# Kernel tuning notes

Measured on AMD Instinct MI355X. Metric: run time of the kernel, lower is better.

Reference implementation:

```python
import jax, jax.numpy as jnp
import numpy as np

N, E, NFEAT, HID, HEADS, NCLASS = 100000, 1600000, 256, 64, 1, 32


def gat_conv(x, src, dst, W, a_src, a_dst, b, H, C, concat):
    n = x.shape[0]
    h = (x @ W).reshape(n, H, C)                      # [N,H,C]
    a_s = (h * a_src).sum(-1)                          # [N,H]
    a_d = (h * a_dst).sum(-1)                          # [N,H]
    e = jax.nn.leaky_relu(a_s[src] + a_d[dst], 0.2)    # [E,H]
    emax = jax.ops.segment_max(e, dst, num_segments=n)
    emax = jnp.where(jnp.isfinite(emax), emax, 0.0)
    ex = jnp.exp(e - emax[dst])
    denom = jax.ops.segment_sum(ex, dst, num_segments=n)
    alpha = ex / (denom[dst] + 1e-16)                  # segment softmax over in-edges of dst
    msg = h[src] * alpha[:, :, None]                   # [E,H,C]
    out = jax.ops.segment_sum(msg, dst, num_segments=n)
    out = out.reshape(n, H * C) if concat else out.mean(axis=1)
    return out + b


def setup_inputs() -> dict:
    key = jax.random.key(0)
    ks = jax.random.split(key, 14)
    x = jax.random.normal(ks[0], (N, NFEAT), dtype=jnp.float32)
    edge_index = jax.random.randint(ks[1], (2, E), 0, N, dtype=jnp.int64)
    s = 0.05
    return {
        'x': x, 'edge_index': edge_index,
        'W1': jax.random.normal(ks[2], (NFEAT, HEADS * HID), jnp.float32) * s,
        'as1': jax.random.normal(ks[3], (HEADS, HID), jnp.float32) * s,
        'ad1': jax.random.normal(ks[4], (HEADS, HID), jnp.float32) * s,
        'b1': jnp.zeros((HEADS * HID,), jnp.float32),
        'W2': jax.random.normal(ks[5], (HEADS * HID, HEADS * HID), jnp.float32) * s,
        'as2': jax.random.normal(ks[6], (HEADS, HID), jnp.float32) * s,
        'ad2': jax.random.normal(ks[7], (HEADS, HID), jnp.float32) * s,
        'b2': jnp.zeros((HEADS * HID,), jnp.float32),
        'W3': jax.random.normal(ks[8], (HEADS * HID, HEADS * NCLASS), jnp.float32) * s,
        'as3': jax.random.normal(ks[9], (HEADS, NCLASS), jnp.float32) * s,
        'ad3': jax.random.normal(ks[10], (HEADS, NCLASS), jnp.float32) * s,
        'b3': jnp.zeros((NCLASS,), jnp.float32),
    }


def reference(x, edge_index, W1, as1, ad1, b1, W2, as2, ad2, b2, W3, as3, ad3, b3):
    # add self loops (PyG GATConv add_self_loops=True)
    loop = jnp.arange(N, dtype=edge_index.dtype)
    src = jnp.concatenate([edge_index[0], loop])
    dst = jnp.concatenate([edge_index[1], loop])
    out = jax.nn.leaky_relu(gat_conv(x, src, dst, W1, as1, ad1, b1, HEADS, HID, True), 0.01)
    out = jax.nn.leaky_relu(gat_conv(out, src, dst, W2, as2, ad2, b2, HEADS, HID, True), 0.01)
    out = gat_conv(out, src, dst, W3, as3, ad3, b3, HEADS, NCLASS, False)
    return out
```

## Files before the change

### kernel.cpp

```cpp
#include <hip/hip_runtime.h>

#define NN 100000
#define NE 1600000
#define NF 256
#define HD 64
#define NC 32

#define BKS 8
#define NBK ((NN + 255) >> 8)
#define CHUNK 4096
#define NBLK ((NE + CHUNK - 1) / CHUNK)

__device__ __forceinline__ float lrelu02(float x) { return fmaxf(x, 0.2f * x); }

typedef __attribute__((ext_vector_type(8))) short bf16x8;
typedef __attribute__((ext_vector_type(4))) float f32x4;
typedef __attribute__((ext_vector_type(4))) _Float16 f16x4;

__device__ __forceinline__ unsigned short f2bf(float f) {
    unsigned int u = __float_as_uint(f);
    unsigned int r = u + 0x7FFFu + ((u >> 16) & 1u);
    return (unsigned short)(r >> 16);
}
__device__ __forceinline__ float bf2f(unsigned short s) {
    return __uint_as_float(((unsigned int)s) << 16);
}
__device__ __forceinline__ void split4(float4 v, uint2& hi, uint2& lo) {
    unsigned short h0 = f2bf(v.x), h1 = f2bf(v.y), h2 = f2bf(v.z), h3 = f2bf(v.w);
    unsigned short l0 = f2bf(v.x - bf2f(h0)), l1 = f2bf(v.y - bf2f(h1));
    unsigned short l2 = f2bf(v.z - bf2f(h2)), l3 = f2bf(v.w - bf2f(h3));
    hi.x = (unsigned int)h0 | ((unsigned int)h1 << 16);
    hi.y = (unsigned int)h2 | ((unsigned int)h3 << 16);
    lo.x = (unsigned int)l0 | ((unsigned int)l1 << 16);
    lo.y = (unsigned int)l2 | ((unsigned int)l3 << 16);
}


__global__ __launch_bounds__(256) void bucket_hist(const int* __restrict__ dst, int* __restrict__ gcnt) {
    __shared__ int hist[NBK];
    int tid = threadIdx.x;
    for (int i = tid; i < NBK; i += 256) hist[i] = 0;
    __syncthreads();
    int base = blockIdx.x * CHUNK;
    #pragma unroll
    for (int k = 0; k < CHUNK / 256; k++) {
        int i = base + k * 256 + tid;
        if (i < NE) atomicAdd(&hist[dst[i] >> BKS], 1);
    }
    __syncthreads();
    for (int i = tid; i < NBK; i += 256) if (hist[i]) atomicAdd(&gcnt[i], hist[i]);
}

__global__ void bucket_scan(const int* __restrict__ gcnt, int* __restrict__ gbase, int* __restrict__ gcur) {
    __shared__ int sh[512];
    int tid = threadIdx.x;
    int v = (tid < NBK) ? gcnt[tid] : 0;
    sh[tid] = v;
    __syncthreads();
    for (int d = 1; d < 512; d <<= 1) {
        int t = (tid >= d) ? sh[tid - d] : 0;
        __syncthreads();
        sh[tid] += t;
        __syncthreads();
    }
    if (tid < NBK) { int ex = sh[tid] - v; gbase[tid] = ex; gcur[tid] = ex; }
}

__global__ __launch_bounds__(256) void bin_edges(const int* __restrict__ src, const int* __restrict__ dst,
                                                 int* __restrict__ gcur, int2* __restrict__ ebuf) {
    __shared__ int hist[NBK];
    __shared__ int excl[NBK];
    __shared__ int runbase[NBK];
    __shared__ int ssum[256];
    __shared__ int2 sorted[CHUNK];
    int tid = threadIdx.x;
    int base = blockIdx.x * CHUNK;
    int n = NE - base; if (n > CHUNK) n = CHUNK;

    for (int i = tid; i < NBK; i += 256) hist[i] = 0;
    __syncthreads();

    int2 ed[CHUNK / 256];
    int bk[CHUNK / 256];
    #pragma unroll
    for (int k = 0; k < CHUNK / 256; k++) {
        int i = base + k * 256 + tid;
        if (i < NE) {
            ed[k] = make_int2(src[i], dst[i]);
            bk[k] = ed[k].y >> BKS;
            atomicAdd(&hist[bk[k]], 1);
        } else bk[k] = -1;
    }
    __syncthreads();
    int h0 = (2 * tid < NBK) ? hist[2 * tid] : 0;
    int h1 = (2 * tid + 1 < NBK) ? hist[2 * tid + 1] : 0;
    ssum[tid] = h0 + h1;
    __syncthreads();
    for (int d = 1; d < 256; d <<= 1) {
        int t = (tid >= d) ? ssum[tid - d] : 0;
        __syncthreads();
        ssum[tid] += t;
        __syncthreads();
    }
    int pref = ssum[tid] - (h0 + h1);
    if (2 * tid < NBK) excl[2 * tid] = pref;
    if (2 * tid + 1 < NBK) excl[2 * tid + 1] = pref + h0;
    for (int b = tid; b < NBK; b += 256) {
        int c = hist[b];
        runbase[b] = c ? atomicAdd(&gcur[b], c) : 0;
    }
    __syncthreads();
    #pragma unroll
    for (int k = 0; k < CHUNK / 256; k++) {
        if (bk[k] >= 0) {
            int r = atomicAdd(&excl[bk[k]], 1);
            sorted[r] = ed[k];
        }
    }
    __syncthreads();
    for (int i = tid; i < n; i += 256) {
        int2 e = sorted[i];
        int b = e.y >> BKS;
        int local_rank = i - (excl[b] - hist[b]);
        ebuf[runbase[b] + local_rank] = e;
    }
}

__global__ __launch_bounds__(256) void bucket_csr(const int2* __restrict__ ebuf, const int* __restrict__ gbase,
                                                  const int* __restrict__ gcnt,
                                                  int* __restrict__ offs, int* __restrict__ csr) {
    __shared__ int hist[256], cur[256], ssum[256];
    int b = blockIdx.x, tid = threadIdx.x;
    int ebeg = gbase[b], cnt = gcnt[b];
    int node0 = b << BKS;
    hist[tid] = 0;
    __syncthreads();
    for (int i = ebeg + tid; i < ebeg + cnt; i += 256)
        atomicAdd(&hist[ebuf[i].y & 255], 1);
    __syncthreads();
    int v = hist[tid];
    ssum[tid] = v;
    __syncthreads();
    for (int d = 1; d < 256; d <<= 1) {
        int t = (tid >= d) ? ssum[tid - d] : 0;
        __syncthreads();
        ssum[tid] += t;
        __syncthreads();
    }
    int ex = ebeg + ssum[tid] - v;
    cur[tid] = ex;
    int nnode = NN - node0; if (nnode > 256) nnode = 256;
    if (tid < nnode) offs[node0 + tid] = ex;
    if (b == NBK - 1 && tid == nnode - 1) offs[NN] = ebeg + cnt;
    __syncthreads();
    for (int i = ebeg + tid; i < ebeg + cnt; i += 256) {
        int2 e = ebuf[i];
        int pos = atomicAdd(&cur[e.y & 255], 1);
        csr[pos] = e.x;
    }
}


template <int CIN, int COUT>
__global__ __launch_bounds__(256) void mfma_gemm(const float* __restrict__ in, const float* __restrict__ W,
                                                 const float* __restrict__ a_s, const float* __restrict__ a_d,
                                                 _Float16* __restrict__ hout, float* __restrict__ asv,
                                                 float* __restrict__ adv) {
    const int KC  = 32;
    const int BM  = 128;
    const int NCT = COUT / 16;
    const int NCH = CIN / KC;
    const int TPC = 256 / COUT;
    const int KPER = KC / TPC;

    __shared__ unsigned short Ah[2][4 * BM * 8];
    __shared__ unsigned short Al[2][4 * BM * 8];
    __shared__ unsigned short Bh[2][4 * COUT * 8];
    __shared__ unsigned short Bl[2][4 * COUT * 8];

    int tid  = threadIdx.x;
    int lane = tid & 63;
    int wave = tid >> 6;
    int fr = lane & 15;
    int kg = lane >> 4;
    int n0base = blockIdx.x * BM;

    int wcol = tid % COUT;
    int kseg = tid / COUT;
    int kb   = kseg * KPER;
    int kgW  = kb >> 3;
    int kofW = kb & 7;

    float4 xr[4];
    float  wreg[KPER];

    f32x4 acc[2][NCT];
    #pragma unroll
    for (int rt = 0; rt < 2; rt++)
        #pragma unroll
        for (int ct = 0; ct < NCT; ct++) acc[rt][ct] = (f32x4){0.f, 0.f, 0.f, 0.f};

    auto load_regs = [&](int k0) {
        #pragma unroll
        for (int i = 0; i < 4; i++) {
            int f = tid + i * 256;
            int row = f >> 3, q = f & 7;
            int gn = n0base + row;
            xr[i] = make_float4(0.f, 0.f, 0.f, 0.f);
            if (gn < NN) xr[i] = *(const float4*)&in[(size_t)gn * CIN + k0 + q * 4];
        }
        #pragma unroll
        for (int j = 0; j < KPER; j++)
            wreg[j] = W[(size_t)(k0 + kb + j) * COUT + wcol];
    };

    auto write_lds = [&](int buf) {
        #pragma unroll
        for (int i = 0; i < 4; i++) {
            int f = tid + i * 256;
            int row = f >> 3, q = f & 7;
            int akg = q >> 1, off = (q & 1) * 4;
            uint2 hi, lo;
            split4(xr[i], hi, lo);
            *(uint2*)&Ah[buf][(akg * BM + row) * 8 + off] = hi;
            *(uint2*)&Al[buf][(akg * BM + row) * 8 + off] = lo;
        }
        unsigned short bh8[8], bl8[8];
        #pragma unroll
        for (int j = 0; j < KPER; j++) {
            bh8[j] = f2bf(wreg[j]);
            bl8[j] = f2bf(wreg[j] - bf2f(bh8[j]));
        }
        if constexpr (KPER == 8) {
            uint4 ph = make_uint4((unsigned)bh8[0] | ((unsigned)bh8[1] << 16), (unsigned)bh8[2] | ((unsigned)bh8[3] << 16),
                                  (unsigned)bh8[4] | ((unsigned)bh8[5] << 16), (unsigned)bh8[6] | ((unsigned)bh8[7] << 16));
            uint4 pl = make_uint4((unsigned)bl8[0] | ((unsigned)bl8[1] << 16), (unsigned)bl8[2] | ((unsigned)bl8[3] << 16),
                                  (unsigned)bl8[4] | ((unsigned)bl8[5] << 16), (unsigned)bl8[6] | ((unsigned)bl8[7] << 16));
            *(uint4*)&Bh[buf][(kgW * COUT + wcol) * 8 + kofW] = ph;
            *(uint4*)&Bl[buf][(kgW * COUT + wcol) * 8 + kofW] = pl;
        } else {
            uint2 ph = make_uint2((unsigned)bh8[0] | ((unsigned)bh8[1] << 16), (unsigned)bh8[2] | ((unsigned)bh8[3] << 16));
            uint2 pl = make_uint2((unsigned)bl8[0] | ((unsigned)bl8[1] << 16), (unsigned)bl8[2] | ((unsigned)bl8[3] << 16));
            *(uint2*)&Bh[buf][(kgW * COUT + wcol) * 8 + kofW] = ph;
            *(uint2*)&Bl[buf][(kgW * COUT + wcol) * 8 + kofW] = pl;
        }
    };

    auto do_mfma = [&](int buf) {
        bf16x8 ah[2], al[2];
        #pragma unroll
        for (int rt = 0; rt < 2; rt++) {
            int row = wave * 32 + rt * 16 + fr;
            ah[rt] = *(const bf16x8*)&Ah[buf][(kg * BM + row) * 8];
            al[rt] = *(const bf16x8*)&Al[buf][(kg * BM + row) * 8];
        }
        #pragma unroll
        for (int ct = 0; ct < NCT; ct++) {
            int col = ct * 16 + fr;
            bf16x8 bh = *(const bf16x8*)&Bh[buf][(kg * COUT + col) * 8];
            bf16x8 bl = *(const bf16x8*)&Bl[buf][(kg * COUT + col) * 8];
            #pragma unroll
            for (int rt = 0; rt < 2; rt++) {
                acc[rt][ct] = __builtin_amdgcn_mfma_f32_16x16x32_bf16(ah[rt], bh, acc[rt][ct], 0, 0, 0);
                acc[rt][ct] = __builtin_amdgcn_mfma_f32_16x16x32_bf16(ah[rt], bl, acc[rt][ct], 0, 0, 0);
                acc[rt][ct] = __builtin_amdgcn_mfma_f32_16x16x32_bf16(al[rt], bh, acc[rt][ct], 0, 0, 0);
            }
        }
    };

    load_regs(0);
    write_lds(0);
    __syncthreads();

    for (int t = 0; t < NCH; t++) {
        int cur = t & 1;
        if (t + 1 < NCH) load_regs((t + 1) * KC);
        do_mfma(cur);
        if (t + 1 < NCH) {
            write_lds(cur ^ 1);
            __syncthreads();
        }
    }

    float As_l[NCT], Ad_l[NCT];
    #pragma unroll
    for (int ct = 0; ct < NCT; ct++) {
        As_l[ct] = a_s[ct * 16 + fr];
        Ad_l[ct] = a_d[ct * 16 + fr];
    }
    #pragma unroll
    for (int rt = 0; rt < 2; rt++) {
        #pragma unroll
        for (int r = 0; r < 4; r++) {
            int row = n0base + wave * 32 + rt * 16 + kg * 4 + r;
            if (row < NN) {
                #pragma unroll
                for (int ct = 0; ct < NCT; ct++)
                    hout[(size_t)row * COUT + ct * 16 + fr] = (_Float16)acc[rt][ct][r];
            }
            float ps = 0.f, pd = 0.f;
            #pragma unroll
            for (int ct = 0; ct < NCT; ct++) {
                ps += acc[rt][ct][r] * As_l[ct];
                pd += acc[rt][ct][r] * Ad_l[ct];
            }
            #pragma unroll
            for (int off = 1; off < 16; off <<= 1) {
                ps += __shfl_xor(ps, off);
                pd += __shfl_xor(pd, off);
            }
            if (fr == 0 && row < NN) { asv[row] = ps; adv[row] = pd; }
        }
    }
}


template <int C, bool ACT>
__global__ __launch_bounds__(256) void gat_agg(const _Float16* __restrict__ h16, const float* __restrict__ asv,
                                               const float* __restrict__ adv, const int* __restrict__ offs,
                                               const int* __restrict__ csr,
                                               const float* __restrict__ bias, float* __restrict__ out) {
    const int LPR = C / 4;
    const int G = 64 / LPR;
    const f16x4* hh = (const f16x4*)h16;
    int lane = threadIdx.x & 63;
    int v = blockIdx.x * 4 + (threadIdx.x >> 6);
    int beg = offs[v], end = offs[v + 1];
    int g = lane / LPR, r = lane % LPR;
    float adv_v = adv[v];

    float4 acc = {0.f, 0.f, 0.f, 0.f};
    float dsum = 0.f;
    #pragma unroll 4
    for (int e = beg + g; e < end; e += G) {
        int s = csr[e];
        float ww = __expf(lrelu02(asv[s] + adv_v));
        f16x4 hv = hh[(size_t)s * LPR + r];
        dsum += ww;
        acc.x += ww * (float)hv[0]; acc.y += ww * (float)hv[1];
        acc.z += ww * (float)hv[2]; acc.w += ww * (float)hv[3];
    }
    #pragma unroll
    for (int off = LPR; off < 64; off <<= 1) {
        acc.x += __shfl_xor(acc.x, off);
        acc.y += __shfl_xor(acc.y, off);
        acc.z += __shfl_xor(acc.z, off);
        acc.w += __shfl_xor(acc.w, off);
        dsum += __shfl_xor(dsum, off);
    }
    if (g == 0) {
        float selfw = __expf(lrelu02(asv[v] + adv_v));
        f16x4 hs = hh[(size_t)v * LPR + r];
        acc.x += selfw * (float)hs[0]; acc.y += selfw * (float)hs[1];
        acc.z += selfw * (float)hs[2]; acc.w += selfw * (float)hs[3];
        dsum += selfw;
        float inv = 1.f / (dsum + 1e-16f);
        float4 bb = ((const float4*)bias)[r];
        float4 o;
        o.x = acc.x * inv + bb.x; o.y = acc.y * inv + bb.y;
        o.z = acc.z * inv + bb.z; o.w = acc.w * inv + bb.w;
        if (ACT) {
            o.x = fmaxf(o.x, 0.01f * o.x); o.y = fmaxf(o.y, 0.01f * o.y);
            o.z = fmaxf(o.z, 0.01f * o.z); o.w = fmaxf(o.w, 0.01f * o.w);
        }
        ((float4*)out)[(size_t)v * LPR + r] = o;
    }
}


extern "C" void kernel_launch(void* const* d_in, const int* in_sizes, int n_in,
                              void* d_out, int out_size, void* d_ws, size_t ws_size,
                              hipStream_t stream) {
    const float* x   = (const float*)d_in[0];
    const int*   ei  = (const int*)d_in[1];
    const float* W1  = (const float*)d_in[2];
    const float* as1 = (const float*)d_in[3];
    const float* ad1 = (const float*)d_in[4];
    const float* b1  = (const float*)d_in[5];
    const float* W2  = (const float*)d_in[6];
    const float* as2 = (const float*)d_in[7];
    const float* ad2 = (const float*)d_in[8];
    const float* b2  = (const float*)d_in[9];
    const float* W3  = (const float*)d_in[10];
    const float* as3 = (const float*)d_in[11];
    const float* ad3 = (const float*)d_in[12];
    const float* b3  = (const float*)d_in[13];
    float* out = (float*)d_out;

    const int* srcp = ei;
    const int* dstp = ei + NE;

    char* w = (char*)d_ws;
    _Float16* h16 = (_Float16*)w;  w += sizeof(_Float16) * (size_t)NN * HD;
    float* featB = (float*)w;   w += sizeof(float) * (size_t)NN * HD;
    float* asv   = (float*)w;   w += sizeof(float) * NN;
    float* advv  = (float*)w;   w += sizeof(float) * NN;
    int* offs    = (int*)w;     w += sizeof(int) * (NN + 1);
    int* csr     = (int*)w;     w += sizeof(int) * (size_t)NE;
    int2* ebuf   = (int2*)w;    w += sizeof(int2) * (size_t)NE;
    int* gcnt    = (int*)w;     w += sizeof(int) * NBK;
    int* gbase   = (int*)w;     w += sizeof(int) * NBK;
    int* gcur    = (int*)w;     w += sizeof(int) * NBK;

    const int GBM = (NN + 127) / 128;

    hipMemsetAsync(gcnt, 0, sizeof(int) * NBK, stream);
    bucket_hist<<<NBLK, 256, 0, stream>>>(dstp, gcnt);
    bucket_scan<<<1, 512, 0, stream>>>(gcnt, gbase, gcur);
    bin_edges<<<NBLK, 256, 0, stream>>>(srcp, dstp, gcur, ebuf);
    bucket_csr<<<NBK, 256, 0, stream>>>(ebuf, gbase, gcnt, offs, csr);

    mfma_gemm<NF, HD><<<GBM, 256, 0, stream>>>(x, W1, as1, ad1, h16, asv, advv);
    gat_agg<HD, true><<<NN / 4, 256, 0, stream>>>(h16, asv, advv, offs, csr, b1, featB);

    mfma_gemm<HD, HD><<<GBM, 256, 0, stream>>>(featB, W2, as2, ad2, h16, asv, advv);
    gat_agg<HD, true><<<NN / 4, 256, 0, stream>>>(h16, asv, advv, offs, csr, b2, featB);

    mfma_gemm<HD, NC><<<GBM, 256, 0, stream>>>(featB, W3, as3, ad3, h16, asv, advv);
    gat_agg<NC, false><<<NN / 4, 256, 0, stream>>>(h16, asv, advv, offs, csr, b3, out);
}
```

Before: 434.3 us.

## Load GEMM A-tile directly into MFMA registers, bypassing LDS, with smaller blocks

The MFMA GEMM no longer stages the input rows through shared memory. Each lane loads its own 8 fp32 values per row tile straight from global memory and splits them into bf16 hi/lo fragments in registers. Only the weight tile still goes through double-buffered LDS. Blocks shrink to 128 threads covering 64 rows, doubling the grid. This removes LDS writes, reads and their bank traffic for A, at the cost of less coalesced global loads (each lane reads 32 bytes at a row stride).

Result: no change. 427.6 us (-1.5%).

```diff
diff --git a/kernel.cpp b/kernel.cpp
--- a/kernel.cpp
+++ b/kernel.cpp
@@ -24,15 +24,6 @@
 }
 __device__ __forceinline__ float bf2f(unsigned short s) {
     return __uint_as_float(((unsigned int)s) << 16);
-}
-__device__ __forceinline__ void split4(float4 v, uint2& hi, uint2& lo) {
-    unsigned short h0 = f2bf(v.x), h1 = f2bf(v.y), h2 = f2bf(v.z), h3 = f2bf(v.w);
-    unsigned short l0 = f2bf(v.x - bf2f(h0)), l1 = f2bf(v.y - bf2f(h1));
-    unsigned short l2 = f2bf(v.z - bf2f(h2)), l3 = f2bf(v.w - bf2f(h3));
-    hi.x = (unsigned int)h0 | ((unsigned int)h1 << 16);
-    hi.y = (unsigned int)h2 | ((unsigned int)h3 << 16);
-    lo.x = (unsigned int)l0 | ((unsigned int)l1 << 16);
-    lo.y = (unsigned int)l2 | ((unsigned int)l3 << 16);
 }
 
 
@@ -162,19 +153,16 @@
 
 
 template <int CIN, int COUT>
-__global__ __launch_bounds__(256) void mfma_gemm(const float* __restrict__ in, const float* __restrict__ W,
+__global__ __launch_bounds__(128) void mfma_gemm(const float* __restrict__ in, const float* __restrict__ W,
                                                  const float* __restrict__ a_s, const float* __restrict__ a_d,
                                                  _Float16* __restrict__ hout, float* __restrict__ asv,
                                                  float* __restrict__ adv) {
     const int KC  = 32;
-    const int BM  = 128;
+    const int BM  = 64;
     const int NCT = COUT / 16;
     const int NCH = CIN / KC;
-    const int TPC = 256 / COUT;
-    const int KPER = KC / TPC;
-
-    __shared__ unsigned short Ah[2][4 * BM * 8];
-    __shared__ unsigned short Al[2][4 * BM * 8];
+    const int SPT = (4 * COUT) / 128;
+
     __shared__ unsigned short Bh[2][4 * COUT * 8];
     __shared__ unsigned short Bl[2][4 * COUT * 8];
 
@@ -184,15 +172,19 @@
     int fr = lane & 15;
     int kg = lane >> 4;
     int n0base = blockIdx.x * BM;
-
-    int wcol = tid % COUT;
-    int kseg = tid / COUT;
-    int kb   = kseg * KPER;
-    int kgW  = kb >> 3;
-    int kofW = kb & 7;
+    int rbase  = n0base + wave * 32;
+
+    int scol[SPT], skg[SPT];
+    #pragma unroll
+    for (int i = 0; i < SPT; i++) {
+        int s = tid + i * 128;
+        scol[i] = s % COUT;
+        skg[i]  = s / COUT;
+    }
 
     float4 xr[4];
-    float  wreg[KPER];
+    float  wv[SPT][8];
+    bf16x8 ah[2], al[2];
 
     f32x4 acc[2][NCT];
     #pragma unroll
@@ -200,60 +192,56 @@
         #pragma unroll
         for (int ct = 0; ct < NCT; ct++) acc[rt][ct] = (f32x4){0.f, 0.f, 0.f, 0.f};
 
-    auto load_regs = [&](int k0) {
-        #pragma unroll
-        for (int i = 0; i < 4; i++) {
-            int f = tid + i * 256;
-            int row = f >> 3, q = f & 7;
-            int gn = n0base + row;
-            xr[i] = make_float4(0.f, 0.f, 0.f, 0.f);
-            if (gn < NN) xr[i] = *(const float4*)&in[(size_t)gn * CIN + k0 + q * 4];
-        }
-        #pragma unroll
-        for (int j = 0; j < KPER; j++)
-            wreg[j] = W[(size_t)(k0 + kb + j) * COUT + wcol];
+    auto load_A = [&](int k0) {
+        #pragma unroll
+        for (int rt = 0; rt < 2; rt++) {
+            int gr = rbase + rt * 16 + fr;
+            if (gr < NN) {
+                const float* p = &in[(size_t)gr * CIN + k0 + kg * 8];
+                xr[rt * 2 + 0] = *(const float4*)p;
+                xr[rt * 2 + 1] = *(const float4*)(p + 4);
+            } else {
+                xr[rt * 2 + 0] = make_float4(0.f, 0.f, 0.f, 0.f);
+                xr[rt * 2 + 1] = make_float4(0.f, 0.f, 0.f, 0.f);
+            }
+        }
     };
-
-    auto write_lds = [&](int buf) {
-        #pragma unroll
-        for (int i = 0; i < 4; i++) {
-            int f = tid + i * 256;
-            int row = f >> 3, q = f & 7;
-            int akg = q >> 1, off = (q & 1) * 4;
-            uint2 hi, lo;
-            split4(xr[i], hi, lo);
-            *(uint2*)&Ah[buf][(akg * BM + row) * 8 + off] = hi;
-            *(uint2*)&Al[buf][(akg * BM + row) * 8 + off] = lo;
-        }
-        unsigned short bh8[8], bl8[8];
-        #pragma unroll
-        for (int j = 0; j < KPER; j++) {
-            bh8[j] = f2bf(wreg[j]);
-            bl8[j] = f2bf(wreg[j] - bf2f(bh8[j]));
-        }
-        if constexpr (KPER == 8) {
-            uint4 ph = make_uint4((unsigned)bh8[0] | ((unsigned)bh8[1] << 16), (unsigned)bh8[2] | ((unsigned)bh8[3] << 16),
-                                  (unsigned)bh8[4] | ((unsigned)bh8[5] << 16), (unsigned)bh8[6] | ((unsigned)bh8[7] << 16));
-            uint4 pl = make_uint4((unsigned)bl8[0] | ((unsigned)bl8[1] << 16), (unsigned)bl8[2] | ((unsigned)bl8[3] << 16),
-                                  (unsigned)bl8[4] | ((unsigned)bl8[5] << 16), (unsigned)bl8[6] | ((unsigned)bl8[7] << 16));
-            *(uint4*)&Bh[buf][(kgW * COUT + wcol) * 8 + kofW] = ph;
-            *(uint4*)&Bl[buf][(kgW * COUT + wcol) * 8 + kofW] = pl;
-        } else {
-            uint2 ph = make_uint2((unsigned)bh8[0] | ((unsigned)bh8[1] << 16), (unsigned)bh8[2] | ((unsigned)bh8[3] << 16));
-            uint2 pl = make_uint2((unsigned)bl8[0] | ((unsigned)bl8[1] << 16), (unsigned)bl8[2] | ((unsigned)bl8[3] << 16));
-            *(uint2*)&Bh[buf][(kgW * COUT + wcol) * 8 + kofW] = ph;
-            *(uint2*)&Bl[buf][(kgW * COUT + wcol) * 8 + kofW] = pl;
+    auto conv_A = [&]() {
+        #pragma unroll
+        for (int rt = 0; rt < 2; rt++) {
+            const float* v = (const float*)&xr[rt * 2];
+            unsigned short hs[8], ls[8];
+            #pragma unroll
+            for (int j = 0; j < 8; j++) {
+                hs[j] = f2bf(v[j]);
+                ls[j] = f2bf(v[j] - bf2f(hs[j]));
+            }
+            ah[rt] = *(bf16x8*)hs;
+            al[rt] = *(bf16x8*)ls;
         }
     };
-
+    auto load_B = [&](int k0) {
+        #pragma unroll
+        for (int i = 0; i < SPT; i++)
+            #pragma unroll
+            for (int j = 0; j < 8; j++)
+                wv[i][j] = W[(size_t)(k0 + skg[i] * 8 + j) * COUT + scol[i]];
+    };
+    auto write_B = [&](int buf) {
+        #pragma unroll
+        for (int i = 0; i < SPT; i++) {
+            unsigned short hs[8], ls[8];
+            #pragma unroll
+            for (int j = 0; j < 8; j++) {
+                hs[j] = f2bf(wv[i][j]);
+                ls[j] = f2bf(wv[i][j] - bf2f(hs[j]));
+            }
+            int idx = (skg[i] * COUT + scol[i]) * 8;
+            *(uint4*)&Bh[buf][idx] = *(uint4*)hs;
+            *(uint4*)&Bl[buf][idx] = *(uint4*)ls;
+        }
+    };
     auto do_mfma = [&](int buf) {
-        bf16x8 ah[2], al[2];
-        #pragma unroll
-        for (int rt = 0; rt < 2; rt++) {
-            int row = wave * 32 + rt * 16 + fr;
-            ah[rt] = *(const bf16x8*)&Ah[buf][(kg * BM + row) * 8];
-            al[rt] = *(const bf16x8*)&Al[buf][(kg * BM + row) * 8];
-        }
         #pragma unroll
         for (int ct = 0; ct < NCT; ct++) {
             int col = ct * 16 + fr;
@@ -268,16 +256,22 @@
         }
     };
 
-    load_regs(0);
-    write_lds(0);
+    load_A(0);
+    load_B(0);
+    conv_A();
+    write_B(0);
     __syncthreads();
 
     for (int t = 0; t < NCH; t++) {
         int cur = t & 1;
-        if (t + 1 < NCH) load_regs((t + 1) * KC);
+        if (t + 1 < NCH) {
+            load_A((t + 1) * KC);
+            load_B((t + 1) * KC);
+        }
         do_mfma(cur);
         if (t + 1 < NCH) {
-            write_lds(cur ^ 1);
+            write_B(cur ^ 1);
+            conv_A();
             __syncthreads();
         }
     }
@@ -292,7 +286,7 @@
     for (int rt = 0; rt < 2; rt++) {
         #pragma unroll
         for (int r = 0; r < 4; r++) {
-            int row = n0base + wave * 32 + rt * 16 + kg * 4 + r;
+            int row = rbase + rt * 16 + kg * 4 + r;
             if (row < NN) {
                 #pragma unroll
                 for (int ct = 0; ct < NCT; ct++)
@@ -402,7 +396,7 @@
     int* gbase   = (int*)w;     w += sizeof(int) * NBK;
     int* gcur    = (int*)w;     w += sizeof(int) * NBK;
 
-    const int GBM = (NN + 127) / 128;
+    const int GBM = (NN + 63) / 64;
 
     hipMemsetAsync(gcnt, 0, sizeof(int) * NBK, stream);
     bucket_hist<<<NBLK, 256, 0, stream>>>(dstp, gcnt);
@@ -410,12 +404,12 @@
     bin_edges<<<NBLK, 256, 0, stream>>>(srcp, dstp, gcur, ebuf);
     bucket_csr<<<NBK, 256, 0, stream>>>(ebuf, gbase, gcnt, offs, csr);
 
-    mfma_gemm<NF, HD><<<GBM, 256, 0, stream>>>(x, W1, as1, ad1, h16, asv, advv);
+    mfma_gemm<NF, HD><<<GBM, 128, 0, stream>>>(x, W1, as1, ad1, h16, asv, advv);
     gat_agg<HD, true><<<NN / 4, 256, 0, stream>>>(h16, asv, advv, offs, csr, b1, featB);
 
-    mfma_gemm<HD, HD><<<GBM, 256, 0, stream>>>(featB, W2, as2, ad2, h16, asv, advv);
+    mfma_gemm<HD, HD><<<GBM, 128, 0, stream>>>(featB, W2, as2, ad2, h16, asv, advv);
     gat_agg<HD, true><<<NN / 4, 256, 0, stream>>>(h16, asv, advv, offs, csr, b2, featB);
 
-    mfma_gemm<HD, NC><<<GBM, 256, 0, stream>>>(featB, W3, as3, ad3, h16, asv, advv);
+    mfma_gemm<HD, NC><<<GBM, 128, 0, stream>>>(featB, W3, as3, ad3, h16, asv, advv);
     gat_agg<NC, false><<<NN / 4, 256, 0, stream>>>(h16, asv, advv, offs, csr, b3, out);
 }
```
